# Kernel optimization log

Hardware: AMD Instinct MI355X
Metric: run time of the kernel (lower is better)

Reference implementation:

```python
import jax, jax.numpy as jnp
import numpy as np

B, S, D_IN, D_OUT = 4, 2048, 4096, 4096

def setup_inputs() -> dict:
    key = jax.random.key(0)
    k1, k2, k3 = jax.random.split(key, 3)
    x = jax.random.normal(k1, (B, S, D_IN), dtype=jnp.float32)
    quantized_weight = jax.random.randint(k2, (D_OUT, D_IN), 0, 127, dtype=jnp.int32)
    weight_zero_point = jax.random.randint(k3, (1,), 0, 10, dtype=jnp.int32)
    weight_scale = jnp.full((1,), 0.01, dtype=jnp.float32)
    bias = jnp.zeros((D_OUT,), dtype=jnp.float32)
    return {"x": x, "quantized_weight": quantized_weight,
            "weight_zero_point": weight_zero_point,
            "weight_scale": weight_scale, "bias": bias}

def reference(x, quantized_weight, weight_zero_point, weight_scale, bias):
    # dequantize_weight: (q - zp) * scale, then F.linear(x, W, b) = x @ W.T + b
    w = (quantized_weight.astype(jnp.float32)
         - weight_zero_point.astype(jnp.float32)) * weight_scale  # [D_OUT, D_IN]
    return jnp.einsum('bsi,oi->bso', x, w) + bias
```

## Files before the change

kernel.cpp:

```cpp
#include <hip/hip_runtime.h>


typedef __bf16 bf16x8 __attribute__((ext_vector_type(8)));
typedef float  f32x4  __attribute__((ext_vector_type(4)));


__global__ __launch_bounds__(256) void cvt_x_bf16(
    const float4* __restrict__ x, uint4* __restrict__ o, int n8) {
  int i = blockIdx.x * 256 + threadIdx.x;
  if (i >= n8) return;
  float4 a = x[2 * i];
  float4 b = x[2 * i + 1];
  union { __bf16 h[8]; uint4 u; } r;
  r.h[0] = (__bf16)a.x; r.h[1] = (__bf16)a.y;
  r.h[2] = (__bf16)a.z; r.h[3] = (__bf16)a.w;
  r.h[4] = (__bf16)b.x; r.h[5] = (__bf16)b.y;
  r.h[6] = (__bf16)b.z; r.h[7] = (__bf16)b.w;
  o[i] = r.u;
}

__global__ __launch_bounds__(256) void cvt_w_bf16(
    const int4* __restrict__ q, const int* __restrict__ zp,
    uint4* __restrict__ o, int n8) {
  int i = blockIdx.x * 256 + threadIdx.x;
  if (i >= n8) return;
  int z = zp[0];
  int4 a = q[2 * i];
  int4 b = q[2 * i + 1];
  union { __bf16 h[8]; uint4 u; } r;
  r.h[0] = (__bf16)(float)(a.x - z); r.h[1] = (__bf16)(float)(a.y - z);
  r.h[2] = (__bf16)(float)(a.z - z); r.h[3] = (__bf16)(float)(a.w - z);
  r.h[4] = (__bf16)(float)(b.x - z); r.h[5] = (__bf16)(float)(b.y - z);
  r.h[6] = (__bf16)(float)(b.z - z); r.h[7] = (__bf16)(float)(b.w - z);
  o[i] = r.u;
}


#define SLOT_A(d, h) ((((d) * 2 + (h)) << 14))
#define SLOT_B(d, h) ((1 << 16) + (((d) * 2 + (h)) << 14))

#define STAGE(gbase, ldsOff, h, s)                                            \
  do {                                                                        \
    const char* g_ = (gbase) + (size_t)(h) * 128 * K2 + (size_t)(s) * 128;    \
    __builtin_amdgcn_global_load_lds(                                         \
        (const __attribute__((address_space(1))) void*)(g_),                  \
        (__attribute__((address_space(3))) void*)(smem + (ldsOff) + wave * 2048), \
        16, 0, 0);                                                            \
    __builtin_amdgcn_global_load_lds(                                         \
        (const __attribute__((address_space(1))) void*)(g_ + 64),             \
        (__attribute__((address_space(3))) void*)(smem + (ldsOff) + wave * 2048 + 1024), \
        16, 0, 0);                                                            \
  } while (0)

#define LOAD_AF(d, qm)                                                        \
  do {                                                                        \
    _Pragma("unroll") for (int mf = 0; mf < 4; ++mf)                          \
    _Pragma("unroll") for (int kh = 0; kh < 2; ++kh)                          \
        af[mf][kh] = *(const bf16x8*)(smem + SLOT_A(d, qm) +                  \
            (((wr * 4 + mf) * 2 + kh) << 10) + innerOff);                     \
  } while (0)

#define LOAD_BF(dst, d, qn)                                                   \
  do {                                                                        \
    _Pragma("unroll") for (int nf = 0; nf < 2; ++nf)                          \
    _Pragma("unroll") for (int kh = 0; kh < 2; ++kh)                          \
        dst[nf][kh] = *(const bf16x8*)(smem + SLOT_B(d, qn) +                 \
            (((wc * 2 + nf) * 2 + kh) << 10) + innerOff);                     \
  } while (0)

#define MFMA_QUAD(qm, qn, BFR)                                                \
  do {                                                                        \
    __builtin_amdgcn_s_setprio(1);                                            \
    _Pragma("unroll") for (int kh = 0; kh < 2; ++kh)                          \
    _Pragma("unroll") for (int mf = 0; mf < 4; ++mf)                          \
    _Pragma("unroll") for (int nf = 0; nf < 2; ++nf)                          \
        acc[qm][qn][mf][nf] = __builtin_amdgcn_mfma_f32_16x16x32_bf16(        \
            af[mf][kh], BFR[nf][kh], acc[qm][qn][mf][nf], 0, 0, 0);           \
    __builtin_amdgcn_s_setprio(0);                                            \
  } while (0)

#define TILE2(t, d, e, FULL, PRE)                                             \
  do {                                                                        \
                                                    \
    LOAD_AF(d, 0);                                                            \
    LOAD_BF(bf0, d, 0);                                                       \
    if (PRE) STAGE(Abase, SLOT_A(e, 1), 1, (t) + 1);                          \
    LOAD_BF(bf1, d, 1);                                                       \
    MFMA_QUAD(0, 0, bf0);                                                     \
    MFMA_QUAD(0, 1, bf1);                                                     \
    asm volatile("s_waitcnt vmcnt(8)");                                       \
    __builtin_amdgcn_s_barrier();                                             \
                                                    \
    LOAD_AF(d, 1);                                                            \
    if (FULL) { STAGE(Abase, SLOT_A(d, 0), 0, (t) + 2);                       \
                STAGE(Bbase, SLOT_B(d, 0), 0, (t) + 2);                       \
                STAGE(Bbase, SLOT_B(d, 1), 1, (t) + 2); }                     \
    MFMA_QUAD(1, 1, bf1);                                                     \
    MFMA_QUAD(1, 0, bf0);                                                     \
    if (FULL) { asm volatile("s_waitcnt vmcnt(8)"); }                         \
    else      { asm volatile("s_waitcnt vmcnt(0)"); }                         \
    __builtin_amdgcn_s_barrier();                                             \
  } while (0)

__global__ __launch_bounds__(512, 2) void gemm256(
    const __bf16* __restrict__ A, const __bf16* __restrict__ Bw,
    const float* __restrict__ scale, const float* __restrict__ bias,
    float* __restrict__ C) {
  extern __shared__ char smem[];

  constexpr int N = 4096, K = 4096;
  constexpr size_t K2 = (size_t)K * 2;

  const int tid  = threadIdx.x;
  const int wave = tid >> 6;
  const int lane = tid & 63;
  const int fr   = lane & 15;
  const int quad = lane >> 4;
  const int wr   = wave >> 2;
  const int wc   = wave & 3;

  const int nwg = gridDim.x;
  const int cpx = nwg >> 3;
  const int swzid = ((int)blockIdx.x & 7) * cpx + ((int)blockIdx.x >> 3);
  const int nbx = N >> 8;
  const int bx = swzid % nbx;
  const int by = swzid / nbx;

  const int rowLane = wave * 16 + (lane >> 2);
  const int colLane = ((lane & 3) << 4) ^ (((lane >> 3) & 3) << 4);
  const char* Abase = (const char*)A  + (size_t)(by * 256 + rowLane) * K2 + colLane;
  const char* Bbase = (const char*)Bw + (size_t)(bx * 256 + rowLane) * K2 + colLane;

  const int innerOff = (fr << 6) | ((quad << 4) ^ (((fr >> 1) & 3) << 4));

  f32x4 acc[2][2][4][2] = {};
  bf16x8 af[4][2], bf0[2][2], bf1[2][2];

  const int nt = K >> 6;
  (void)nt;

  STAGE(Abase, SLOT_A(0, 0), 0, 0);
  STAGE(Bbase, SLOT_B(0, 0), 0, 0);
  STAGE(Bbase, SLOT_B(0, 1), 1, 0);
  STAGE(Abase, SLOT_A(0, 1), 1, 0);
  STAGE(Abase, SLOT_A(1, 0), 0, 1);
  STAGE(Bbase, SLOT_B(1, 0), 0, 1);
  STAGE(Bbase, SLOT_B(1, 1), 1, 1);
  asm volatile("s_waitcnt vmcnt(8)");
  __builtin_amdgcn_s_barrier();

  for (int tt = 0; tt < 62; tt += 2) {
    TILE2(tt,     0, 1, 1, 1);
    TILE2(tt + 1, 1, 0, 1, 1);
  }
  TILE2(62, 0, 1, 0, 1);
  TILE2(63, 1, 0, 0, 0);

  const float s = scale[0];
#pragma unroll
  for (int qm = 0; qm < 2; ++qm)
#pragma unroll
    for (int mf = 0; mf < 4; ++mf) {
      const int row0 = by * 256 + qm * 128 + wr * 64 + mf * 16 + quad * 4;
#pragma unroll
      for (int qn = 0; qn < 2; ++qn)
#pragma unroll
        for (int nf = 0; nf < 2; ++nf) {
          const int col = bx * 256 + qn * 128 + wc * 32 + nf * 16 + fr;
          const float bv = bias[col];
          float* cp = C + (size_t)row0 * N + col;
#pragma unroll
          for (int r = 0; r < 4; ++r)
            cp[(size_t)r * N] = s * acc[qm][qn][mf][nf][r] + bv;
        }
    }
}


extern "C" void kernel_launch(void* const* d_in, const int* in_sizes, int n_in,
                              void* d_out, int out_size, void* d_ws, size_t ws_size,
                              hipStream_t stream) {
  const int M = 8192, N = 4096, K = 4096;

  const float* x    = (const float*)d_in[0];
  const int*   qw   = (const int*)d_in[1];
  const int*   zp   = (const int*)d_in[2];
  const float* sc   = (const float*)d_in[3];
  const float* bias = (const float*)d_in[4];
  float* out = (float*)d_out;

  __bf16* x_bf = (__bf16*)d_ws;
  __bf16* w_bf = (__bf16*)((char*)d_ws + (size_t)M * K * sizeof(__bf16));

  {
    int n8 = (M * K) / 8;
    cvt_x_bf16<<<n8 / 256, 256, 0, stream>>>((const float4*)x, (uint4*)x_bf, n8);
  }
  {
    int n8 = (N * K) / 8;
    cvt_w_bf16<<<n8 / 256, 256, 0, stream>>>((const int4*)qw, zp, (uint4*)w_bf, n8);
  }

  static bool attr_set = false;
  if (!attr_set) {
    hipFuncSetAttribute((const void*)gemm256,
                        hipFuncAttributeMaxDynamicSharedMemorySize, 131072);
    attr_set = true;
  }
  gemm256<<<dim3(512), dim3(512), 131072, stream>>>(x_bf, w_bf, sc, bias, out);
}
```

Before: 480.9 us.

## Switch GEMM to 32x32x16 MFMA with k-split LDS staging

Replaces the 16x16x32 bf16 MFMA tiles with 32x32x16 MFMA, so each wave computes a 128x64 sub-tile held as 4x2 32x32 accumulators. LDS staging is reorganized to split each 64-wide K tile into two 32-wide halves rather than two M/N halves, with new swizzled fragment offsets and a rewritten prefetch and wait schedule. The larger MFMA shape aims to cut LDS fragment reads per FLOP and raise matrix-core efficiency, at the cost of a new LDS addressing scheme and tighter pipeline wait counts that could stall or conflict.

```diff
diff --git a/kernel.cpp b/kernel.cpp
--- a/kernel.cpp
+++ b/kernel.cpp
@@ -2,7 +2,7 @@
 
 
 typedef __bf16 bf16x8 __attribute__((ext_vector_type(8)));
-typedef float  f32x4  __attribute__((ext_vector_type(4)));
+typedef float  f32x16 __attribute__((ext_vector_type(16)));
 
 
 __global__ __launch_bounds__(256) void cvt_x_bf16(
@@ -36,69 +36,69 @@
 }
 
 
-#define SLOT_A(d, h) ((((d) * 2 + (h)) << 14))
-#define SLOT_B(d, h) ((1 << 16) + (((d) * 2 + (h)) << 14))
-
-#define STAGE(gbase, ldsOff, h, s)                                            \
-  do {                                                                        \
-    const char* g_ = (gbase) + (size_t)(h) * 128 * K2 + (size_t)(s) * 128;    \
+#define SLOT32_A(d, kh) ((((d) * 2 + (kh)) << 14))
+#define SLOT32_B(d, kh) ((1 << 16) + (((d) * 2 + (kh)) << 14))
+
+#define WAITVM_(n) asm volatile("s_waitcnt vmcnt(" #n ")")
+#define WAITVM(n) WAITVM_(n)
+
+#define STAGE32(gbase, ldsOff, kh, s)                                         \
+  do {                                                                        \
+    const char* g_ = (gbase) + (size_t)(kh) * 64 + (size_t)(s) * 128;         \
     __builtin_amdgcn_global_load_lds(                                         \
         (const __attribute__((address_space(1))) void*)(g_),                  \
         (__attribute__((address_space(3))) void*)(smem + (ldsOff) + wave * 2048), \
         16, 0, 0);                                                            \
     __builtin_amdgcn_global_load_lds(                                         \
-        (const __attribute__((address_space(1))) void*)(g_ + 64),             \
+        (const __attribute__((address_space(1))) void*)(g_ + 16 * K2),        \
         (__attribute__((address_space(3))) void*)(smem + (ldsOff) + wave * 2048 + 1024), \
         16, 0, 0);                                                            \
   } while (0)
 
-#define LOAD_AF(d, qm)                                                        \
-  do {                                                                        \
-    _Pragma("unroll") for (int mf = 0; mf < 4; ++mf)                          \
-    _Pragma("unroll") for (int kh = 0; kh < 2; ++kh)                          \
-        af[mf][kh] = *(const bf16x8*)(smem + SLOT_A(d, qm) +                  \
-            (((wr * 4 + mf) * 2 + kh) << 10) + innerOff);                     \
-  } while (0)
-
-#define LOAD_BF(dst, d, qn)                                                   \
+#define LOAD_A32(d, kh)                                                       \
+  do {                                                                        \
+    _Pragma("unroll") for (int mrf = 0; mrf < 4; ++mrf)                       \
+    _Pragma("unroll") for (int ks2 = 0; ks2 < 2; ++ks2)                       \
+        af[mrf][ks2] = *(const bf16x8*)(smem + SLOT32_A(d, kh) + aSub +       \
+            mrf * 2048 + ((ks2 << 5) ^ kLo));                                 \
+  } while (0)
+
+#define LOAD_B32(d, kh)                                                       \
   do {                                                                        \
     _Pragma("unroll") for (int nf = 0; nf < 2; ++nf)                          \
-    _Pragma("unroll") for (int kh = 0; kh < 2; ++kh)                          \
-        dst[nf][kh] = *(const bf16x8*)(smem + SLOT_B(d, qn) +                 \
-            (((wc * 2 + nf) * 2 + kh) << 10) + innerOff);                     \
-  } while (0)
-
-#define MFMA_QUAD(qm, qn, BFR)                                                \
+    _Pragma("unroll") for (int ks2 = 0; ks2 < 2; ++ks2)                       \
+        bf[nf][ks2] = *(const bf16x8*)(smem + SLOT32_B(d, kh) + bSub +        \
+            nf * 2048 + ((ks2 << 5) ^ kLo));                                  \
+  } while (0)
+
+#define MFMA32()                                                              \
   do {                                                                        \
     __builtin_amdgcn_s_setprio(1);                                            \
-    _Pragma("unroll") for (int kh = 0; kh < 2; ++kh)                          \
-    _Pragma("unroll") for (int mf = 0; mf < 4; ++mf)                          \
+    _Pragma("unroll") for (int ks2 = 0; ks2 < 2; ++ks2)                       \
+    _Pragma("unroll") for (int mrf = 0; mrf < 4; ++mrf)                       \
     _Pragma("unroll") for (int nf = 0; nf < 2; ++nf)                          \
-        acc[qm][qn][mf][nf] = __builtin_amdgcn_mfma_f32_16x16x32_bf16(        \
-            af[mf][kh], BFR[nf][kh], acc[qm][qn][mf][nf], 0, 0, 0);           \
+        acc[mrf][nf] = __builtin_amdgcn_mfma_f32_32x32x16_bf16(               \
+            af[mrf][ks2], bf[nf][ks2], acc[mrf][nf], 0, 0, 0);                \
     __builtin_amdgcn_s_setprio(0);                                            \
   } while (0)
 
-#define TILE2(t, d, e, FULL, PRE)                                             \
-  do {                                                                        \
-                                                    \
-    LOAD_AF(d, 0);                                                            \
-    LOAD_BF(bf0, d, 0);                                                       \
-    if (PRE) STAGE(Abase, SLOT_A(e, 1), 1, (t) + 1);                          \
-    LOAD_BF(bf1, d, 1);                                                       \
-    MFMA_QUAD(0, 0, bf0);                                                     \
-    MFMA_QUAD(0, 1, bf1);                                                     \
-    asm volatile("s_waitcnt vmcnt(8)");                                       \
+#define TILE32(t, d, e, S1, S2)                                               \
+  do {                                                                        \
+                                                                \
+    LOAD_A32(d, 0);                                                           \
+    LOAD_B32(d, 0);                                                           \
+    if (S1) { STAGE32(Abase, SLOT32_A(e, 1), 1, (t) + 1);                     \
+              STAGE32(Bbase, SLOT32_B(e, 1), 1, (t) + 1); }                   \
+    MFMA32();                                                                 \
+    if (S1) { WAITVM(8); } else { WAITVM(0); }                                \
     __builtin_amdgcn_s_barrier();                                             \
-                                                    \
-    LOAD_AF(d, 1);                                                            \
-    if (FULL) { STAGE(Abase, SLOT_A(d, 0), 0, (t) + 2);                       \
-                STAGE(Bbase, SLOT_B(d, 0), 0, (t) + 2);                       \
-                STAGE(Bbase, SLOT_B(d, 1), 1, (t) + 2); }                     \
-    MFMA_QUAD(1, 1, bf1);                                                     \
-    MFMA_QUAD(1, 0, bf0);                                                     \
-    if (FULL) { asm volatile("s_waitcnt vmcnt(8)"); }                         \
-    else      { asm volatile("s_waitcnt vmcnt(0)"); }                         \
+                                                                \
+    LOAD_A32(d, 1);                                                           \
+    LOAD_B32(d, 1);                                                           \
+    if (S2) { STAGE32(Abase, SLOT32_A(d, 0), 0, (t) + 2);                     \
+              STAGE32(Bbase, SLOT32_B(d, 0), 0, (t) + 2); }                   \
+    MFMA32();                                                                 \
+    if (S2) { WAITVM(8); } else if (S1) { WAITVM(4); }                        \
     __builtin_amdgcn_s_barrier();                                             \
   } while (0)
 
@@ -114,8 +114,6 @@
   const int tid  = threadIdx.x;
   const int wave = tid >> 6;
   const int lane = tid & 63;
-  const int fr   = lane & 15;
-  const int quad = lane >> 4;
   const int wr   = wave >> 2;
   const int wc   = wave & 3;
 
@@ -126,54 +124,51 @@
   const int bx = swzid % nbx;
   const int by = swzid / nbx;
 
-  const int rowLane = wave * 16 + (lane >> 2);
+  const int rowLane = wave * 32 + (lane >> 2);
   const int colLane = ((lane & 3) << 4) ^ (((lane >> 3) & 3) << 4);
   const char* Abase = (const char*)A  + (size_t)(by * 256 + rowLane) * K2 + colLane;
   const char* Bbase = (const char*)Bw + (size_t)(bx * 256 + rowLane) * K2 + colLane;
 
-  const int innerOff = (fr << 6) | ((quad << 4) ^ (((fr >> 1) & 3) << 4));
-
-  f32x4 acc[2][2][4][2] = {};
-  bf16x8 af[4][2], bf0[2][2], bf1[2][2];
-
-  const int nt = K >> 6;
-  (void)nt;
-
-  STAGE(Abase, SLOT_A(0, 0), 0, 0);
-  STAGE(Bbase, SLOT_B(0, 0), 0, 0);
-  STAGE(Bbase, SLOT_B(0, 1), 1, 0);
-  STAGE(Abase, SLOT_A(0, 1), 1, 0);
-  STAGE(Abase, SLOT_A(1, 0), 0, 1);
-  STAGE(Bbase, SLOT_B(1, 0), 0, 1);
-  STAGE(Bbase, SLOT_B(1, 1), 1, 1);
-  asm volatile("s_waitcnt vmcnt(8)");
+  const int aSub = (wr * 8 + ((lane >> 4) & 1)) * 1024 + ((lane & 15) << 6);
+  const int bSub = (wc * 4 + ((lane >> 4) & 1)) * 1024 + ((lane & 15) << 6);
+  const int kLo  = (((lane >> 5) & 1) << 4) ^ (((lane >> 1) & 3) << 4);
+
+  f32x16 acc[4][2] = {};
+  bf16x8 af[4][2], bf[2][2];
+
+  STAGE32(Abase, SLOT32_A(0, 0), 0, 0);
+  STAGE32(Bbase, SLOT32_B(0, 0), 0, 0);
+  STAGE32(Abase, SLOT32_A(0, 1), 1, 0);
+  STAGE32(Bbase, SLOT32_B(0, 1), 1, 0);
+  STAGE32(Abase, SLOT32_A(1, 0), 0, 1);
+  STAGE32(Bbase, SLOT32_B(1, 0), 0, 1);
+  WAITVM(8);
   __builtin_amdgcn_s_barrier();
 
   for (int tt = 0; tt < 62; tt += 2) {
-    TILE2(tt,     0, 1, 1, 1);
-    TILE2(tt + 1, 1, 0, 1, 1);
-  }
-  TILE2(62, 0, 1, 0, 1);
-  TILE2(63, 1, 0, 0, 0);
+    TILE32(tt,     0, 1, 1, 1);
+    TILE32(tt + 1, 1, 0, 1, 1);
+  }
+  TILE32(62, 0, 1, 1, 0);
+  TILE32(63, 1, 0, 0, 0);
 
   const float s = scale[0];
 #pragma unroll
-  for (int qm = 0; qm < 2; ++qm)
-#pragma unroll
-    for (int mf = 0; mf < 4; ++mf) {
-      const int row0 = by * 256 + qm * 128 + wr * 64 + mf * 16 + quad * 4;
-#pragma unroll
-      for (int qn = 0; qn < 2; ++qn)
-#pragma unroll
-        for (int nf = 0; nf < 2; ++nf) {
-          const int col = bx * 256 + qn * 128 + wc * 32 + nf * 16 + fr;
-          const float bv = bias[col];
-          float* cp = C + (size_t)row0 * N + col;
-#pragma unroll
-          for (int r = 0; r < 4; ++r)
-            cp[(size_t)r * N] = s * acc[qm][qn][mf][nf][r] + bv;
-        }
+  for (int mrf = 0; mrf < 4; ++mrf) {
+    const int row0 = by * 256 + wr * 128 + mrf * 32 + ((lane >> 5) << 2);
+#pragma unroll
+    for (int nf = 0; nf < 2; ++nf) {
+      const int col = bx * 256 + wc * 64 + nf * 32 + (lane & 31);
+      const float bv = bias[col];
+#pragma unroll
+      for (int g = 0; g < 4; ++g) {
+        float* cp = C + (size_t)(row0 + g * 8) * N + col;
+#pragma unroll
+        for (int rr = 0; rr < 4; ++rr)
+          cp[(size_t)rr * N] = s * acc[mrf][nf][g * 4 + rr] + bv;
+      }
     }
+  }
 }
 
 
```

Measured after the change: 534.8 us. 1.11x slower.
